# Kernel tuning notes

Hardware: AMD Instinct MI355X
Metric: run time of the kernel (lower is better)

Reference implementation:

```python
import jax, jax.numpy as jnp
import numpy as np

EPS = 1e-6

def setup_inputs() -> dict:
    key = jax.random.key(0)
    k1, k2, k3 = jax.random.split(key, 3)
    B, D, T = 4096, 4096, 16
    inputs = jax.random.normal(k1, (B, D), dtype=jnp.float32)
    W = jax.random.normal(k2, (D, T), dtype=jnp.float32)
    W_static = jax.random.normal(k3, (D, T), dtype=jnp.float32)
    return {"inputs": inputs, "W": W, "W_static": W_static}


def _znorm(A):
    # batch z-normalization per column (population std, matching tf.math.reduce_std)
    return (A - A.mean(axis=0)) / (A.std(axis=0) + EPS)


def _pls_scan(X, Ws):
    """Sequential PLS-style deflation: factor i is produced after
    orthogonalizing X against the z-normalized previous factors."""
    B = X.shape[0]
    denom = jnp.asarray(B, X.dtype)
    T = Ws.shape[1]
    cols = [X @ Ws[:, 0:1]]  # [B,1]
    for i in range(1, T):
        C = jnp.concatenate(cols, axis=1)          # [B,i]
        conv = _znorm(C)                           # [B,i]
        beta = (conv.T @ X) / denom                # [i,D]
        lin = X - conv @ beta                      # deflated inputs [B,D]
        cols.append(lin @ Ws[:, i:i + 1])
    return jnp.concatenate(cols, axis=1)           # [B,T]


def reference(inputs, W, W_static):
    # training path of FactorLayer.call
    X = _znorm(inputs)                              # batchnorm of inputs [B,D]
    c_mat = _pls_scan(X, W_static)                  # calculate_cmat with static weights
    B = X.shape[0]
    denom = jnp.asarray(B, X.dtype)
    T = W.shape[1]
    outs = [X @ W[:, 0:1]]
    for i in range(1, T):
        Cs = c_mat[:, :i]
        conv = _znorm(Cs)
        beta = (conv.T @ X) / denom                 # [i,D]
        lin = X - conv @ beta                       # training_run output [B,D]
        outs.append(lin @ W[:, i:i + 1])
    return jnp.concatenate(outs, axis=1)            # [B,T]
```

## Files before the change

kernel.cpp:

```cpp
#include <hip/hip_runtime.h>
#include <stdint.h>


#define BB 4096
#define DD 4096
#define EPSF 1e-6f

#define O_PART    0u
#define O_WSF     1048576u
#define O_GRAMM   1179648u
#define O_YZ      1188608u
#define O_YPART   1319680u

__device__ __forceinline__ int gidx(int a, int b) {
    int lo = a < b ? a : b, hi = a < b ? b : a;
    return lo * 33 + hi;
}

__global__ __launch_bounds__(256, 2)
void kA(const float* __restrict__ in, const float* __restrict__ W,
        const float* __restrict__ Wstat, float* __restrict__ ws) {
    int b = blockIdx.x, t = threadIdx.x;
    int idx = b * 256 + t;
    if (idx < 8960) ws[O_GRAMM + idx] = 0.f;
    {
        int d = idx >> 5, j = idx & 31;
        ws[O_WSF + idx] = (j < 16) ? Wstat[d * 16 + j] : W[d * 16 + (j - 16)];
    }
    int cgk = b & 3, rg = b >> 2;
    int c0 = cgk * 1024 + t * 4, r0 = rg * 32;
    float s0=0.f,s1=0.f,s2=0.f,s3=0.f,q0=0.f,q1=0.f,q2=0.f,q3=0.f;
    #pragma unroll 4
    for (int r = 0; r < 32; ++r) {
        float4 u = *(const float4*)&in[(size_t)(r0 + r) * DD + c0];
        s0 += u.x; q0 += u.x*u.x;  s1 += u.y; q1 += u.y*u.y;
        s2 += u.z; q2 += u.z*u.z;  s3 += u.w; q3 += u.w*u.w;
    }
    float* part = ws + O_PART + (size_t)rg * 8192;
    *(float4*)&part[c0]        = make_float4(s0, s1, s2, s3);
    *(float4*)&part[4096 + c0] = make_float4(q0, q1, q2, q3);
}

__global__ __launch_bounds__(256, 8)
void kB(const float* __restrict__ in, const float* __restrict__ ws,
        float* __restrict__ ypart) {
    __shared__ __align__(16) float tile[64 * 33];
    __shared__ __align__(16) float mu_s[128];
    __shared__ __align__(16) float inv_s[128];
    __shared__ __align__(16) float muinv_s[128];
    int b = blockIdx.x, t = threadIdx.x;
    int dg = b & 31, rg = b >> 5;
    int dbase = dg * 128, rowbase = rg * 64;
    {
        int half = t >> 7, ci = t & 127;
        const float* p0 = ws + O_PART + (size_t)half * 4096 + dbase + ci;
        float a = 0.f;
        #pragma unroll 8
        for (int g = 0; g < 128; ++g) a += p0[(size_t)g * 8192];
        if (half == 0) mu_s[ci] = a * (1.0f / BB);
        __syncthreads();
        if (half == 1) {
            float m = mu_s[ci];
            float var = a * (1.0f / BB) - m * m; if (var < 0.f) var = 0.f;
            float iv = 1.0f / (sqrtf(var) + EPSF);
            inv_s[ci] = iv; muinv_s[ci] = m * iv;
        }
        __syncthreads();
    }
    float acc[8];
    #pragma unroll
    for (int i = 0; i < 8; ++i) acc[i] = 0.f;
    int chunk = t & 7, srow = t >> 3;
    int row = t & 63;
    int jq = __builtin_amdgcn_readfirstlane(t >> 6);
    const float* wsf = ws + O_WSF;
    const float* inp = in + (size_t)(rowbase + srow) * DD + dbase + chunk * 4;
    float4 pf0, pf1;
    pf0 = *(const float4*)(inp);
    pf1 = *(const float4*)(inp + (size_t)32 * DD);
    for (int stage = 0; stage < 4; ++stage) {
        int ds0 = stage * 32;
        float4 iv4 = *(const float4*)&inv_s[ds0 + chunk * 4];
        float4 mi4 = *(const float4*)&muinv_s[ds0 + chunk * 4];
        int b0 = srow * 33 + chunk * 4;
        tile[b0 + 0] = pf0.x * iv4.x - mi4.x;
        tile[b0 + 1] = pf0.y * iv4.y - mi4.y;
        tile[b0 + 2] = pf0.z * iv4.z - mi4.z;
        tile[b0 + 3] = pf0.w * iv4.w - mi4.w;
        int b1 = (srow + 32) * 33 + chunk * 4;
        tile[b1 + 0] = pf1.x * iv4.x - mi4.x;
        tile[b1 + 1] = pf1.y * iv4.y - mi4.y;
        tile[b1 + 2] = pf1.z * iv4.z - mi4.z;
        tile[b1 + 3] = pf1.w * iv4.w - mi4.w;
        __syncthreads();
        if (stage < 3) {
            pf0 = *(const float4*)(inp + (stage + 1) * 32);
            pf1 = *(const float4*)(inp + (size_t)32 * DD + (stage + 1) * 32);
        }
        const float* trow = tile + row * 33;
        #pragma unroll 4
        for (int dl = 0; dl < 32; ++dl) {
            float xs = trow[dl];
            const float* wr = wsf + (size_t)(dbase + ds0 + dl) * 32 + jq * 8;
            #pragma unroll
            for (int j = 0; j < 8; ++j) acc[j] += xs * wr[j];
        }
        __syncthreads();
    }
    float* dst = ypart + ((size_t)dg * BB + rowbase + row) * 32 + jq * 8;
    *(float4*)(dst + 0) = make_float4(acc[0], acc[1], acc[2], acc[3]);
    *(float4*)(dst + 4) = make_float4(acc[4], acc[5], acc[6], acc[7]);
}

__global__ __launch_bounds__(256, 2)
void kC(float* __restrict__ ws) {
    __shared__ float yz_s[8 * 34];
    int b = blockIdx.x, t = threadIdx.x;
    int rowbase = b * 8;
    int r = t >> 5, c = t & 31;
    const float* yp = ws + O_YPART;
    size_t off = (size_t)(rowbase + r) * 32 + c;
    float s = 0.f;
    #pragma unroll
    for (int dg = 0; dg < 32; ++dg) s += yp[(size_t)dg * (BB * 32) + off];
    ws[O_YZ + off] = s;
    yz_s[r * 34 + c] = s;
    if (c == 0) yz_s[r * 34 + 32] = 1.0f;
    __syncthreads();
    float* gm = ws + O_GRAMM + (size_t)(b & 7) * 1120;
    for (int p = t; p < 561; p += 256) {
        int i = 0, rem = p;
        while (rem >= 33 - i) { rem -= 33 - i; ++i; }
        int j = i + rem;
        float a2 = 0.f;
        #pragma unroll
        for (int r2 = 0; r2 < 8; ++r2) a2 += yz_s[r2 * 34 + i] * yz_s[r2 * 34 + j];
        atomicAdd(&gm[i * 33 + j], a2);
    }
}

__global__ __launch_bounds__(256, 2)
void kE(const float* __restrict__ ws, float* __restrict__ out) {
    __shared__ __align__(16) float yzs[64 * 36];
    __shared__ float GA[17 * 17], gz[17 * 16], v[15][17], gad[15][16],
                     gzd[15][16], gu[17], u[17], st[2], wm[17 * 16];
    int b = blockIdx.x, t = threadIdx.x;
    int rowbase = b * 64;
    const float4* src = (const float4*)(ws + O_YZ) + (size_t)rowbase * 8;
    #pragma unroll
    for (int k = 0; k < 2; ++k) {
        int idx = k * 256 + t;
        float4 f = src[idx];
        int row = idx >> 3, c4 = (idx & 7) * 4;
        yzs[row * 36 + c4 + 0] = f.x; yzs[row * 36 + c4 + 1] = f.y;
        yzs[row * 36 + c4 + 2] = f.z; yzs[row * 36 + c4 + 3] = f.w;
    }
    const float* gm = ws + O_GRAMM;
    for (int idx = t; idx < 17 * 17; idx += 256) {
        int p = idx / 17, q = idx % 17;
        int gi = gidx(p < 16 ? p : 32, q < 16 ? q : 32);
        float s = 0.f;
        #pragma unroll
        for (int m = 0; m < 8; ++m) s += gm[m * 1120 + gi];
        GA[idx] = s;
    }
    for (int idx = t; idx < 17 * 16; idx += 256) {
        int p = idx / 16, tt = idx % 16;
        int gi = gidx(p < 16 ? p : 32, 16 + tt);
        float s = 0.f;
        #pragma unroll
        for (int m = 0; m < 8; ++m) s += gm[m * 1120 + gi];
        gz[idx] = s;
    }
    if (t < 17) u[t] = (t == 0) ? 1.f : 0.f;
    __syncthreads();
    const float invB = 1.0f / BB;
    for (int i = 0; i < 15; ++i) {
        if (t < 17) {
            float s = 0.f;
            for (int q = 0; q < 17; ++q) s += GA[t * 17 + q] * u[q];
            gu[t] = s;
        }
        __syncthreads();
        if (t == 0) {
            float mean = gu[16] * invB, e2 = 0.f;
            for (int p = 0; p < 17; ++p) e2 += u[p] * gu[p];
            e2 *= invB;
            float var = e2 - mean * mean; if (var < 0.f) var = 0.f;
            st[0] = mean; st[1] = 1.0f / (sqrtf(var) + EPSF);
        }
        __syncthreads();
        if (t < 17) v[i][t] = (u[t] - (t == 16 ? st[0] : 0.f)) * st[1];
        __syncthreads();
        if (t < 16) {
            float s = 0.f;
            for (int p = 0; p < 17; ++p) s += v[i][p] * GA[p * 17 + t];
            gad[i][t] = s;
        } else if (t < 32) {
            int tt = t - 16;
            float s = 0.f;
            for (int p = 0; p < 17; ++p) s += v[i][p] * gz[p * 16 + tt];
            gzd[i][tt] = s;
        }
        __syncthreads();
        if (t < 17) {
            float a2 = 0.f;
            for (int j = 0; j <= i; ++j) a2 += v[j][t] * gad[j][i + 1];
            u[t] = ((t == i + 1) ? 1.f : 0.f) - a2 * invB;
        }
        __syncthreads();
    }
    for (int idx = t; idx < 17 * 16; idx += 256) {
        int p = idx / 16, tt = idx % 16;
        float s = 0.f;
        for (int j = 0; j < tt; ++j) s += v[j][p] * gzd[j][tt];
        wm[idx] = s * invB;
    }
    __syncthreads();
    int row = t >> 2, c0 = (t & 3) * 4;
    const float* yr = yzs + row * 36;
    float o[4];
    #pragma unroll
    for (int k = 0; k < 4; ++k) o[k] = yr[16 + c0 + k] - wm[16 * 16 + c0 + k];
    #pragma unroll
    for (int p = 0; p < 16; ++p) {
        float yp = yr[p];
        #pragma unroll
        for (int k = 0; k < 4; ++k) o[k] -= yp * wm[p * 16 + c0 + k];
    }
    *(float4*)&out[(size_t)rowbase * 16 + t * 4] = make_float4(o[0], o[1], o[2], o[3]);
}

extern "C" void kernel_launch(void* const* d_in, const int* in_sizes, int n_in,
                              void* d_out, int out_size, void* d_ws, size_t ws_size,
                              hipStream_t stream) {
    const float* in    = (const float*)d_in[0];
    const float* W     = (const float*)d_in[1];
    const float* Wstat = (const float*)d_in[2];
    float* ws  = (float*)d_ws;
    float* out = (float*)d_out;

    kA<<<dim3(512),  dim3(256), 0, stream>>>(in, W, Wstat, ws);
    kB<<<dim3(2048), dim3(256), 0, stream>>>(in, ws, ws + O_YPART);
    kC<<<dim3(512),  dim3(256), 0, stream>>>(ws);
    kE<<<dim3(64),   dim3(256), 0, stream>>>(ws, out);
}
```

Measured before the change: 155.7 us.

## Fold inverse std into weights and apply mean correction in the Gram stage

A new small kernel reduces the column statistics once and scales the packed weight matrix by each column's inverse std. The main GEMV kernel then uses raw inputs with no per-block statistics reduction and no per-element normalization. The mean contribution is removed algebraically in the final kernel by correcting the Gram entries and the output offset using the column sums. This drops the redundant 128-way partial reduction repeated in every kB block, at the cost of one extra launch. Subtracting the mean after accumulation rather than before may cost some precision.

After: 151.6 us. -2.6%, faster.

```diff
diff --git a/kernel.cpp b/kernel.cpp
--- a/kernel.cpp
+++ b/kernel.cpp
@@ -18,15 +18,10 @@
 }
 
 __global__ __launch_bounds__(256, 2)
-void kA(const float* __restrict__ in, const float* __restrict__ W,
-        const float* __restrict__ Wstat, float* __restrict__ ws) {
+void kA(const float* __restrict__ in, float* __restrict__ ws) {
     int b = blockIdx.x, t = threadIdx.x;
     int idx = b * 256 + t;
     if (idx < 8960) ws[O_GRAMM + idx] = 0.f;
-    {
-        int d = idx >> 5, j = idx & 31;
-        ws[O_WSF + idx] = (j < 16) ? Wstat[d * 16 + j] : W[d * 16 + (j - 16)];
-    }
     int cgk = b & 3, rg = b >> 2;
     int c0 = cgk * 1024 + t * 4, r0 = rg * 32;
     float s0=0.f,s1=0.f,s2=0.f,s3=0.f,q0=0.f,q1=0.f,q2=0.f,q3=0.f;
@@ -41,32 +36,52 @@
     *(float4*)&part[4096 + c0] = make_float4(q0, q1, q2, q3);
 }
 
+__global__ __launch_bounds__(256, 4)
+void kD(const float* __restrict__ W, const float* __restrict__ Wstat,
+        float* __restrict__ ws) {
+    __shared__ float red[32][9], redq[32][9], invs[32];
+    int b = blockIdx.x, t = threadIdx.x;
+    int dbase = b * 32;
+    {
+        int c1 = t & 31, k1 = t >> 5;
+        const float* part = ws + O_PART;
+        float s = 0.f, q = 0.f;
+        #pragma unroll
+        for (int i = 0; i < 16; ++i) {
+            int g = k1 * 16 + i;
+            s += part[(size_t)g * 8192 + dbase + c1];
+            q += part[(size_t)g * 8192 + 4096 + dbase + c1];
+        }
+        red[c1][k1] = s; redq[c1][k1] = q;
+    }
+    __syncthreads();
+    if (t < 32) {
+        float ss = 0.f, qq = 0.f;
+        #pragma unroll
+        for (int i = 0; i < 8; ++i) { ss += red[t][i]; qq += redq[t][i]; }
+        float m = ss * (1.0f / BB);
+        float var = qq * (1.0f / BB) - m * m; if (var < 0.f) var = 0.f;
+        invs[t] = 1.0f / (sqrtf(var) + EPSF);
+    }
+    __syncthreads();
+    {
+        int c2 = t >> 3, j0 = (t & 7) * 4;
+        int d = dbase + c2;
+        float iv = invs[c2];
+        float4 wv = (j0 < 16) ? *(const float4*)&Wstat[d * 16 + j0]
+                              : *(const float4*)&W[d * 16 + (j0 - 16)];
+        *(float4*)&ws[O_WSF + (size_t)d * 32 + j0] =
+            make_float4(wv.x * iv, wv.y * iv, wv.z * iv, wv.w * iv);
+    }
+}
+
 __global__ __launch_bounds__(256, 8)
 void kB(const float* __restrict__ in, const float* __restrict__ ws,
         float* __restrict__ ypart) {
     __shared__ __align__(16) float tile[64 * 33];
-    __shared__ __align__(16) float mu_s[128];
-    __shared__ __align__(16) float inv_s[128];
-    __shared__ __align__(16) float muinv_s[128];
     int b = blockIdx.x, t = threadIdx.x;
     int dg = b & 31, rg = b >> 5;
     int dbase = dg * 128, rowbase = rg * 64;
-    {
-        int half = t >> 7, ci = t & 127;
-        const float* p0 = ws + O_PART + (size_t)half * 4096 + dbase + ci;
-        float a = 0.f;
-        #pragma unroll 8
-        for (int g = 0; g < 128; ++g) a += p0[(size_t)g * 8192];
-        if (half == 0) mu_s[ci] = a * (1.0f / BB);
-        __syncthreads();
-        if (half == 1) {
-            float m = mu_s[ci];
-            float var = a * (1.0f / BB) - m * m; if (var < 0.f) var = 0.f;
-            float iv = 1.0f / (sqrtf(var) + EPSF);
-            inv_s[ci] = iv; muinv_s[ci] = m * iv;
-        }
-        __syncthreads();
-    }
     float acc[8];
     #pragma unroll
     for (int i = 0; i < 8; ++i) acc[i] = 0.f;
@@ -75,23 +90,16 @@
     int jq = __builtin_amdgcn_readfirstlane(t >> 6);
     const float* wsf = ws + O_WSF;
     const float* inp = in + (size_t)(rowbase + srow) * DD + dbase + chunk * 4;
-    float4 pf0, pf1;
-    pf0 = *(const float4*)(inp);
-    pf1 = *(const float4*)(inp + (size_t)32 * DD);
+    float4 pf0 = *(const float4*)(inp);
+    float4 pf1 = *(const float4*)(inp + (size_t)32 * DD);
     for (int stage = 0; stage < 4; ++stage) {
         int ds0 = stage * 32;
-        float4 iv4 = *(const float4*)&inv_s[ds0 + chunk * 4];
-        float4 mi4 = *(const float4*)&muinv_s[ds0 + chunk * 4];
         int b0 = srow * 33 + chunk * 4;
-        tile[b0 + 0] = pf0.x * iv4.x - mi4.x;
-        tile[b0 + 1] = pf0.y * iv4.y - mi4.y;
-        tile[b0 + 2] = pf0.z * iv4.z - mi4.z;
-        tile[b0 + 3] = pf0.w * iv4.w - mi4.w;
+        tile[b0 + 0] = pf0.x; tile[b0 + 1] = pf0.y;
+        tile[b0 + 2] = pf0.z; tile[b0 + 3] = pf0.w;
         int b1 = (srow + 32) * 33 + chunk * 4;
-        tile[b1 + 0] = pf1.x * iv4.x - mi4.x;
-        tile[b1 + 1] = pf1.y * iv4.y - mi4.y;
-        tile[b1 + 2] = pf1.z * iv4.z - mi4.z;
-        tile[b1 + 3] = pf1.w * iv4.w - mi4.w;
+        tile[b1 + 0] = pf1.x; tile[b1 + 1] = pf1.y;
+        tile[b1 + 2] = pf1.z; tile[b1 + 3] = pf1.w;
         __syncthreads();
         if (stage < 3) {
             pf0 = *(const float4*)(inp + (stage + 1) * 32);
@@ -142,10 +150,11 @@
 __global__ __launch_bounds__(256, 2)
 void kE(const float* __restrict__ ws, float* __restrict__ out) {
     __shared__ __align__(16) float yzs[64 * 36];
-    __shared__ float GA[17 * 17], gz[17 * 16], v[15][17], gad[15][16],
+    __shared__ float Sv[33], GA[17 * 17], gz[17 * 16], v[15][17], gad[15][16],
                      gzd[15][16], gu[17], u[17], st[2], wm[17 * 16];
     int b = blockIdx.x, t = threadIdx.x;
     int rowbase = b * 64;
+    const float invB = 1.0f / BB;
     const float4* src = (const float4*)(ws + O_YZ) + (size_t)rowbase * 8;
     #pragma unroll
     for (int k = 0; k < 2; ++k) {
@@ -156,25 +165,38 @@
         yzs[row * 36 + c4 + 2] = f.z; yzs[row * 36 + c4 + 3] = f.w;
     }
     const float* gm = ws + O_GRAMM;
+    if (t < 33) {
+        float s = 0.f;
+        #pragma unroll
+        for (int m = 0; m < 8; ++m) s += gm[m * 1120 + gidx(t, 32)];
+        Sv[t] = s;
+    }
+    __syncthreads();
     for (int idx = t; idx < 17 * 17; idx += 256) {
         int p = idx / 17, q = idx % 17;
-        int gi = gidx(p < 16 ? p : 32, q < 16 ? q : 32);
-        float s = 0.f;
-        #pragma unroll
-        for (int m = 0; m < 8; ++m) s += gm[m * 1120 + gi];
-        GA[idx] = s;
+        float val;
+        if (p < 16 && q < 16) {
+            float raw = 0.f;
+            #pragma unroll
+            for (int m = 0; m < 8; ++m) raw += gm[m * 1120 + gidx(p, q)];
+            val = raw - Sv[p] * Sv[q] * invB;
+        } else if (p == 16 && q == 16) val = (float)BB;
+        else val = 0.f;
+        GA[idx] = val;
     }
     for (int idx = t; idx < 17 * 16; idx += 256) {
         int p = idx / 16, tt = idx % 16;
-        int gi = gidx(p < 16 ? p : 32, 16 + tt);
-        float s = 0.f;
-        #pragma unroll
-        for (int m = 0; m < 8; ++m) s += gm[m * 1120 + gi];
-        gz[idx] = s;
+        float val = 0.f;
+        if (p < 16) {
+            float raw = 0.f;
+            #pragma unroll
+            for (int m = 0; m < 8; ++m) raw += gm[m * 1120 + gidx(p, 16 + tt)];
+            val = raw - Sv[p] * Sv[16 + tt] * invB;
+        }
+        gz[idx] = val;
     }
     if (t < 17) u[t] = (t == 0) ? 1.f : 0.f;
     __syncthreads();
-    const float invB = 1.0f / BB;
     for (int i = 0; i < 15; ++i) {
         if (t < 17) {
             float s = 0.f;
@@ -217,6 +239,12 @@
         wm[idx] = s * invB;
     }
     __syncthreads();
+    if (t < 16) {
+        float adj = Sv[16 + t] * invB;
+        for (int p = 0; p < 16; ++p) adj -= Sv[p] * invB * wm[p * 16 + t];
+        wm[16 * 16 + t] += adj;
+    }
+    __syncthreads();
     int row = t >> 2, c0 = (t & 3) * 4;
     const float* yr = yzs + row * 36;
     float o[4];
@@ -240,7 +268,8 @@
     float* ws  = (float*)d_ws;
     float* out = (float*)d_out;
 
-    kA<<<dim3(512),  dim3(256), 0, stream>>>(in, W, Wstat, ws);
+    kA<<<dim3(512),  dim3(256), 0, stream>>>(in, ws);
+    kD<<<dim3(128),  dim3(256), 0, stream>>>(W, Wstat, ws);
     kB<<<dim3(2048), dim3(256), 0, stream>>>(in, ws, ws + O_YPART);
     kC<<<dim3(512),  dim3(256), 0, stream>>>(ws);
     kE<<<dim3(64),   dim3(256), 0, stream>>>(ws, out);
```
